# Optimization experiments

Hardware: AMD Instinct MI355X
Metric: run time of the kernel (lower is better)

## Reference

```python
import jax, jax.numpy as jnp
import numpy as np

NUM_USERS = 100000
NUM_ITEMS = 100000
D = 128
B = 8192
L = 200  # max history length (padded)
INIT_STD = 0.1


def setup_inputs() -> dict:
    key = jax.random.key(0)
    ks = jax.random.split(key, 10)
    user_ids = jax.random.randint(ks[0], (B,), 0, NUM_USERS)
    item_ids = jax.random.randint(ks[1], (B,), 0, NUM_ITEMS)
    hist_items = jax.random.randint(ks[2], (B, L), 0, NUM_ITEMS)
    hist_len = jax.random.randint(ks[3], (B,), 0, L + 1)  # ragged lengths in [0, L]
    user_emb = INIT_STD * jax.random.normal(ks[4], (NUM_USERS, D), dtype=jnp.float32)
    item_emb = INIT_STD * jax.random.normal(ks[5], (NUM_ITEMS, D), dtype=jnp.float32)
    implicit_emb = INIT_STD * jax.random.normal(ks[6], (NUM_ITEMS, D), dtype=jnp.float32)
    user_bias = jnp.zeros((NUM_USERS,), dtype=jnp.float32)
    item_bias = jnp.zeros((NUM_ITEMS,), dtype=jnp.float32)
    global_bias = jnp.zeros((), dtype=jnp.float32)
    return {
        "user_ids": user_ids,
        "item_ids": item_ids,
        "hist_items": hist_items,
        "hist_len": hist_len,
        "user_emb": user_emb,
        "item_emb": item_emb,
        "implicit_emb": implicit_emb,
        "user_bias": user_bias,
        "item_bias": item_bias,
        "global_bias": global_bias,
    }


def reference(user_ids, item_ids, hist_items, hist_len,
              user_emb, item_emb, implicit_emb, user_bias, item_bias, global_bias):
    # SVD++: r_ui = mu + b_u + b_i + q_i . (p_u + |N(u)|^{-1/2} * sum_{j in N(u)} y_j)
    p_u = user_emb[user_ids]                       # [B, D]
    q_i = item_emb[item_ids]                       # [B, D]
    b_u = user_bias[user_ids]                      # [B]
    b_i = item_bias[item_ids]                      # [B]

    y = implicit_emb[hist_items]                   # [B, L, D] ragged gather (padded)
    mask = (jnp.arange(L)[None, :] < hist_len[:, None]).astype(y.dtype)  # [B, L]
    implicit_sum = jnp.einsum("bld,bl->bd", y, mask)                     # masked segment-sum
    lens = hist_len.astype(y.dtype)
    norm = jnp.where(hist_len > 0, jax.lax.rsqrt(jnp.maximum(lens, 1.0)), 0.0)  # [B]
    enhanced = p_u + norm[:, None] * implicit_sum  # [B, D]

    dot = jnp.sum(enhanced * q_i, axis=-1)         # [B]
    return global_bias + b_u + b_i + dot
```

## Files before the change

kernel.cpp:

```cpp
#include <hip/hip_runtime.h>


#define BB 8192
#define DD 128
#define LL 200
#define IMP8_BYTES 12800000u

#if defined(__has_builtin)
#if __has_builtin(__builtin_amdgcn_sdot4)
#define HAVE_SDOT4 1
#endif
#endif

__device__ __forceinline__ int dot4(int a, int b, int c) {
#ifdef HAVE_SDOT4
    return __builtin_amdgcn_sdot4(a, b, c, false);
#else
    return c + (int)(signed char)(a & 0xff)         * (int)(signed char)(b & 0xff)
             + (int)(signed char)((a >> 8) & 0xff)  * (int)(signed char)((b >> 8) & 0xff)
             + (int)(signed char)((a >> 16) & 0xff) * (int)(signed char)((b >> 16) & 0xff)
             + (a >> 24)                            * (b >> 24);
#endif
}

__device__ __forceinline__ int q4pack(const float4 v) {
    const int a = max(-127, min(127, (int)rintf(v.x * 256.f)));
    const int b = max(-127, min(127, (int)rintf(v.y * 256.f)));
    const int c = max(-127, min(127, (int)rintf(v.z * 256.f)));
    const int d = max(-127, min(127, (int)rintf(v.w * 256.f)));
    return (a & 0xff) | ((b & 0xff) << 8) | ((c & 0xff) << 16) | ((d & 0xff) << 24);
}

__global__ __launch_bounds__(256) void convert_i8(
    const float* __restrict__ in, uint2* __restrict__ out, int n8)
{
    const int i = blockIdx.x * 256 + threadIdx.x;
    if (i >= n8) return;
    const float4 v0 = reinterpret_cast<const float4*>(in)[2 * i];
    const float4 v1 = reinterpret_cast<const float4*>(in)[2 * i + 1];
    uint2 w;
    w.x = (uint)q4pack(v0);
    w.y = (uint)q4pack(v1);
    out[i] = w;
}

__global__ __launch_bounds__(256, 8) void svdpp_wave_i8(
    const int* __restrict__ user_ids,
    const int* __restrict__ item_ids,
    const int* __restrict__ hist_items,
    const int* __restrict__ hist_len,
    const float* __restrict__ user_emb,
    const float* __restrict__ item_emb,
    const signed char* __restrict__ imp8,
    const float* __restrict__ user_bias,
    const float* __restrict__ item_bias,
    const float* __restrict__ global_bias,
    float* __restrict__ out)
{
    const int wid  = blockIdx.x * 4 + (threadIdx.x >> 6);
    if (wid >= BB) return;
    const int lane = threadIdx.x & 63;
    const int e    = lane >> 3;
    const int el   = lane & 7;

    const int b   = wid;
    const int len = hist_len[b];
    const int it  = item_ids[b];
    const int u   = user_ids[b];

    const float* qp = item_emb + (size_t)it * DD + el * 16;
    int4 qq;
    qq.x = q4pack(*reinterpret_cast<const float4*>(qp));
    qq.y = q4pack(*reinterpret_cast<const float4*>(qp + 4));
    qq.z = q4pack(*reinterpret_cast<const float4*>(qp + 8));
    qq.w = q4pack(*reinterpret_cast<const float4*>(qp + 12));

    const int* __restrict__ hrow = hist_items + (size_t)b * LL;

    int acc = 0;
    int l = e;
    for (; l + 8 < len; l += 16) {
        const int j0 = hrow[l];
        const int j1 = hrow[l + 8];
        const int4 w0 = *reinterpret_cast<const int4*>(imp8 + (size_t)j0 * DD + el * 16);
        const int4 w1 = *reinterpret_cast<const int4*>(imp8 + (size_t)j1 * DD + el * 16);
        acc = dot4(w0.x, qq.x, acc);
        acc = dot4(w0.y, qq.y, acc);
        acc = dot4(w0.z, qq.z, acc);
        acc = dot4(w0.w, qq.w, acc);
        acc = dot4(w1.x, qq.x, acc);
        acc = dot4(w1.y, qq.y, acc);
        acc = dot4(w1.z, qq.z, acc);
        acc = dot4(w1.w, qq.w, acc);
    }
    if (l < len) {
        const int j = hrow[l];
        const int4 w = *reinterpret_cast<const int4*>(imp8 + (size_t)j * DD + el * 16);
        acc = dot4(w.x, qq.x, acc);
        acc = dot4(w.y, qq.y, acc);
        acc = dot4(w.z, qq.z, acc);
        acc = dot4(w.w, qq.w, acc);
    }

    acc += __shfl_xor(acc, 1, 64);
    acc += __shfl_xor(acc, 2, 64);
    acc += __shfl_xor(acc, 4, 64);
    acc += __shfl_xor(acc, 8, 64);
    acc += __shfl_xor(acc, 16, 64);
    acc += __shfl_xor(acc, 32, 64);

    const float2 pv = *reinterpret_cast<const float2*>(user_emb + (size_t)u  * DD + lane * 2);
    const float2 qv = *reinterpret_cast<const float2*>(item_emb + (size_t)it * DD + lane * 2);
    float pd = pv.x * qv.x + pv.y * qv.y;
    pd += __shfl_xor(pd, 1, 64);
    pd += __shfl_xor(pd, 2, 64);
    pd += __shfl_xor(pd, 4, 64);
    pd += __shfl_xor(pd, 8, 64);
    pd += __shfl_xor(pd, 16, 64);
    pd += __shfl_xor(pd, 32, 64);

    if (lane == 0) {
        const float nr = (len > 0) ? rsqrtf((float)len) : 0.f;
        out[b] = global_bias[0] + user_bias[u] + item_bias[it] + pd
               + nr * ((float)acc * (1.f / 65536.f));
    }
}

__global__ __launch_bounds__(256) void svdpp_fp32_kernel(
    const int* __restrict__ user_ids,
    const int* __restrict__ item_ids,
    const int* __restrict__ hist_items,
    const int* __restrict__ hist_len,
    const float* __restrict__ user_emb,
    const float* __restrict__ item_emb,
    const float* __restrict__ implicit_emb,
    const float* __restrict__ user_bias,
    const float* __restrict__ item_bias,
    const float* __restrict__ global_bias,
    float* __restrict__ out)
{
    const int b    = blockIdx.x;
    const int tid  = threadIdx.x;
    const int w    = tid >> 6;
    const int lane = tid & 63;
    const int half = lane >> 5;
    const int sub  = (w << 1) | half;
    const int d0   = (lane & 31) << 2;

    const int len = hist_len[b];
    const int it  = item_ids[b];
    const float4 q = *reinterpret_cast<const float4*>(item_emb + (size_t)it * DD + d0);
    const int* __restrict__ hrow = hist_items + (size_t)b * LL;

    float4 acc = make_float4(0.f, 0.f, 0.f, 0.f);
    int l = sub;
    for (; l + 8 < len; l += 16) {
        const int j0 = hrow[l];
        const int j1 = hrow[l + 8];
        const float4 y0 = *reinterpret_cast<const float4*>(implicit_emb + (size_t)j0 * DD + d0);
        const float4 y1 = *reinterpret_cast<const float4*>(implicit_emb + (size_t)j1 * DD + d0);
        acc.x += y0.x; acc.y += y0.y; acc.z += y0.z; acc.w += y0.w;
        acc.x += y1.x; acc.y += y1.y; acc.z += y1.z; acc.w += y1.w;
    }
    if (l < len) {
        const int j = hrow[l];
        const float4 y = *reinterpret_cast<const float4*>(implicit_emb + (size_t)j * DD + d0);
        acc.x += y.x; acc.y += y.y; acc.z += y.z; acc.w += y.w;
    }

    acc.x += __shfl_xor(acc.x, 32, 64);
    acc.y += __shfl_xor(acc.y, 32, 64);
    acc.z += __shfl_xor(acc.z, 32, 64);
    acc.w += __shfl_xor(acc.w, 32, 64);

    float s = q.x * acc.x + q.y * acc.y + q.z * acc.z + q.w * acc.w;
    s += __shfl_down(s, 16, 64);
    s += __shfl_down(s, 8, 64);
    s += __shfl_down(s, 4, 64);
    s += __shfl_down(s, 2, 64);
    s += __shfl_down(s, 1, 64);

    __shared__ float partial[4];
    if (lane == 0) partial[w] = s;
    __syncthreads();

    if (w == 0) {
        const int u = user_ids[b];
        const float4 p = *reinterpret_cast<const float4*>(user_emb + (size_t)u * DD + d0);
        float bs = p.x * q.x + p.y * q.y + p.z * q.z + p.w * q.w;
        bs += __shfl_down(bs, 16, 64);
        bs += __shfl_down(bs, 8, 64);
        bs += __shfl_down(bs, 4, 64);
        bs += __shfl_down(bs, 2, 64);
        bs += __shfl_down(bs, 1, 64);
        if (lane == 0) {
            const float S = partial[0] + partial[1] + partial[2] + partial[3];
            const float nr = (len > 0) ? rsqrtf((float)len) : 0.f;
            out[b] = global_bias[0] + user_bias[u] + item_bias[it] + bs + nr * S;
        }
    }
}

extern "C" void kernel_launch(void* const* d_in, const int* in_sizes, int n_in,
                              void* d_out, int out_size, void* d_ws, size_t ws_size,
                              hipStream_t stream) {
    const int*   user_ids     = (const int*)d_in[0];
    const int*   item_ids     = (const int*)d_in[1];
    const int*   hist_items   = (const int*)d_in[2];
    const int*   hist_len     = (const int*)d_in[3];
    const float* user_emb     = (const float*)d_in[4];
    const float* item_emb     = (const float*)d_in[5];
    const float* implicit_emb = (const float*)d_in[6];
    const float* user_bias    = (const float*)d_in[7];
    const float* item_bias    = (const float*)d_in[8];
    const float* global_bias  = (const float*)d_in[9];
    float* out = (float*)d_out;

    if (ws_size >= (size_t)IMP8_BYTES) {
        const int n8 = 1600000;
        convert_i8<<<(n8 + 255) / 256, 256, 0, stream>>>(
            implicit_emb, (uint2*)d_ws, n8);
        svdpp_wave_i8<<<BB / 4, 256, 0, stream>>>(
            user_ids, item_ids, hist_items, hist_len,
            user_emb, item_emb, (const signed char*)d_ws,
            user_bias, item_bias, global_bias, out);
    } else {
        svdpp_fp32_kernel<<<BB, 256, 0, stream>>>(
            user_ids, item_ids, hist_items, hist_len,
            user_emb, item_emb, implicit_emb,
            user_bias, item_bias, global_bias, out);
    }
}
```

Baseline: 33.42 us.

## Split each row's history across four waves with shared-memory reduction

Assigns one 256-thread block per batch row instead of one wave per row, with the four waves striding over the history and combining their int8 dot-product partials through shared memory. The aim is more parallelism in flight per row and better latency hiding for the random embedding gathers, and less tail imbalance from ragged lengths. It adds a block barrier, redundant q-vector loads and packing in every wave, and four times as many waves launched.

```diff
diff --git a/kernel.cpp b/kernel.cpp
--- a/kernel.cpp
+++ b/kernel.cpp
@@ -44,7 +44,7 @@
     out[i] = w;
 }
 
-__global__ __launch_bounds__(256, 8) void svdpp_wave_i8(
+__global__ __launch_bounds__(256, 8) void svdpp_block_i8(
     const int* __restrict__ user_ids,
     const int* __restrict__ item_ids,
     const int* __restrict__ hist_items,
@@ -57,13 +57,15 @@
     const float* __restrict__ global_bias,
     float* __restrict__ out)
 {
-    const int wid  = blockIdx.x * 4 + (threadIdx.x >> 6);
-    if (wid >= BB) return;
-    const int lane = threadIdx.x & 63;
+    const int b    = blockIdx.x;
+    const int tid  = threadIdx.x;
+    const int w    = tid >> 6;
+    const int lane = tid & 63;
     const int e    = lane >> 3;
     const int el   = lane & 7;
 
-    const int b   = wid;
+    __shared__ int wsum[4];
+
     const int len = hist_len[b];
     const int it  = item_ids[b];
     const int u   = user_ids[b];
@@ -78,10 +80,10 @@
     const int* __restrict__ hrow = hist_items + (size_t)b * LL;
 
     int acc = 0;
-    int l = e;
-    for (; l + 8 < len; l += 16) {
+    int l = (w << 3) | e;
+    for (; l + 32 < len; l += 64) {
         const int j0 = hrow[l];
-        const int j1 = hrow[l + 8];
+        const int j1 = hrow[l + 32];
         const int4 w0 = *reinterpret_cast<const int4*>(imp8 + (size_t)j0 * DD + el * 16);
         const int4 w1 = *reinterpret_cast<const int4*>(imp8 + (size_t)j1 * DD + el * 16);
         acc = dot4(w0.x, qq.x, acc);
@@ -95,11 +97,11 @@
     }
     if (l < len) {
         const int j = hrow[l];
-        const int4 w = *reinterpret_cast<const int4*>(imp8 + (size_t)j * DD + el * 16);
-        acc = dot4(w.x, qq.x, acc);
-        acc = dot4(w.y, qq.y, acc);
-        acc = dot4(w.z, qq.z, acc);
-        acc = dot4(w.w, qq.w, acc);
+        const int4 ww = *reinterpret_cast<const int4*>(imp8 + (size_t)j * DD + el * 16);
+        acc = dot4(ww.x, qq.x, acc);
+        acc = dot4(ww.y, qq.y, acc);
+        acc = dot4(ww.z, qq.z, acc);
+        acc = dot4(ww.w, qq.w, acc);
     }
 
     acc += __shfl_xor(acc, 1, 64);
@@ -108,21 +110,25 @@
     acc += __shfl_xor(acc, 8, 64);
     acc += __shfl_xor(acc, 16, 64);
     acc += __shfl_xor(acc, 32, 64);
-
-    const float2 pv = *reinterpret_cast<const float2*>(user_emb + (size_t)u  * DD + lane * 2);
-    const float2 qv = *reinterpret_cast<const float2*>(item_emb + (size_t)it * DD + lane * 2);
-    float pd = pv.x * qv.x + pv.y * qv.y;
-    pd += __shfl_xor(pd, 1, 64);
-    pd += __shfl_xor(pd, 2, 64);
-    pd += __shfl_xor(pd, 4, 64);
-    pd += __shfl_xor(pd, 8, 64);
-    pd += __shfl_xor(pd, 16, 64);
-    pd += __shfl_xor(pd, 32, 64);
-
-    if (lane == 0) {
-        const float nr = (len > 0) ? rsqrtf((float)len) : 0.f;
-        out[b] = global_bias[0] + user_bias[u] + item_bias[it] + pd
-               + nr * ((float)acc * (1.f / 65536.f));
+    if (lane == 0) wsum[w] = acc;
+    __syncthreads();
+
+    if (tid < 64) {
+        const float2 pv = *reinterpret_cast<const float2*>(user_emb + (size_t)u  * DD + tid * 2);
+        const float2 qv = *reinterpret_cast<const float2*>(item_emb + (size_t)it * DD + tid * 2);
+        float pd = pv.x * qv.x + pv.y * qv.y;
+        pd += __shfl_xor(pd, 1, 64);
+        pd += __shfl_xor(pd, 2, 64);
+        pd += __shfl_xor(pd, 4, 64);
+        pd += __shfl_xor(pd, 8, 64);
+        pd += __shfl_xor(pd, 16, 64);
+        pd += __shfl_xor(pd, 32, 64);
+        if (tid == 0) {
+            const int Si = wsum[0] + wsum[1] + wsum[2] + wsum[3];
+            const float nr = (len > 0) ? rsqrtf((float)len) : 0.f;
+            out[b] = global_bias[0] + user_bias[u] + item_bias[it] + pd
+                   + nr * ((float)Si * (1.f / 65536.f));
+        }
     }
 }
 
@@ -220,7 +226,7 @@
         const int n8 = 1600000;
         convert_i8<<<(n8 + 255) / 256, 256, 0, stream>>>(
             implicit_emb, (uint2*)d_ws, n8);
-        svdpp_wave_i8<<<BB / 4, 256, 0, stream>>>(
+        svdpp_block_i8<<<BB, 256, 0, stream>>>(
             user_ids, item_ids, hist_items, hist_len,
             user_emb, item_emb, (const signed char*)d_ws,
             user_bias, item_bias, global_bias, out);
```

Measured after the change: 36.80 us. 1.1x slower.
